# Kernel optimization log

Measured on AMD Instinct MI355X. Metric: run time of the kernel, lower is better.

The kernel has to match this reference:

```python
import jax, jax.numpy as jnp
import numpy as np

HIDDEN = 2048
N_HEADS = 16
N_KV_HEADS = 4
HEAD_DIM = HIDDEN // N_HEADS  # 128
N_GROUPS = N_HEADS // N_KV_HEADS  # 4
ROPE_THETA = 10000.0
B, S = 2, 2048


def setup_inputs() -> dict:
    key = jax.random.key(0)
    k1, k2, k3, k4, k5, k6 = jax.random.split(key, 6)
    hidden_states = jax.random.normal(k1, (B, S, HIDDEN), dtype=jnp.float32)
    position_ids = jnp.sort(jax.random.randint(k2, (B, S), 0, S), axis=-1).astype(jnp.int32)
    scale = 0.02
    Wq = jax.random.normal(k3, (HIDDEN, N_HEADS * HEAD_DIM), dtype=jnp.float32) * scale
    Wk = jax.random.normal(k4, (HIDDEN, N_KV_HEADS * HEAD_DIM), dtype=jnp.float32) * scale
    Wv = jax.random.normal(k5, (HIDDEN, N_KV_HEADS * HEAD_DIM), dtype=jnp.float32) * scale
    Wo = jax.random.normal(k6, (HIDDEN, HIDDEN), dtype=jnp.float32) * scale
    return {"hidden_states": hidden_states, "position_ids": position_ids,
            "Wq": Wq, "Wk": Wk, "Wv": Wv, "Wo": Wo}


def _rotate_half(x):
    x1, x2 = jnp.split(x, 2, axis=-1)
    return jnp.concatenate([-x2, x1], axis=-1)


def _rope_cos_sin(position_ids, dtype):
    # inv_freq: [HEAD_DIM/2]
    inv_freq = 1.0 / (ROPE_THETA ** (jnp.arange(0, HEAD_DIM, 2, dtype=jnp.float32) / HEAD_DIM))
    # freqs per position: [B, S, HEAD_DIM/2] -> duplicated to [B, S, HEAD_DIM]
    freqs = position_ids.astype(jnp.float32)[..., None] * inv_freq  # [B,S,Dh/2]
    emb = jnp.concatenate([freqs, freqs], axis=-1)  # [B,S,Dh]
    cos = jnp.cos(emb)[:, None, :, :].astype(dtype)  # [B,1,S,Dh]
    sin = jnp.sin(emb)[:, None, :, :].astype(dtype)
    return cos, sin


def reference(hidden_states, position_ids, Wq, Wk, Wv, Wo):
    b, s, _ = hidden_states.shape
    dtype = hidden_states.dtype
    q = (hidden_states @ Wq).reshape(b, s, N_HEADS, HEAD_DIM).transpose(0, 2, 1, 3)      # [B,Hq,S,Dh]
    k = (hidden_states @ Wk).reshape(b, s, N_KV_HEADS, HEAD_DIM).transpose(0, 2, 1, 3)   # [B,Hkv,S,Dh]
    v = (hidden_states @ Wv).reshape(b, s, N_KV_HEADS, HEAD_DIM).transpose(0, 2, 1, 3)

    cos, sin = _rope_cos_sin(position_ids, dtype)
    q = q * cos + _rotate_half(q) * sin
    k = k * cos + _rotate_half(k) * sin

    # repeat_kv: [B,Hkv,S,Dh] -> [B,Hq,S,Dh] (repeat-interleave along head axis)
    k = jnp.repeat(k, N_GROUPS, axis=1)
    v = jnp.repeat(v, N_GROUPS, axis=1)

    scores = jnp.einsum('bhqd,bhkd->bhqk', q, k) / jnp.sqrt(jnp.asarray(HEAD_DIM, dtype))
    # causal additive mask
    causal = jnp.tril(jnp.ones((s, s), dtype=bool))
    scores = jnp.where(causal[None, None], scores, jnp.asarray(-1e9, dtype))
    probs = jax.nn.softmax(scores, axis=-1)
    attn = jnp.einsum('bhqk,bhkd->bhqd', probs, v)  # [B,Hq,S,Dh]
    attn = attn.transpose(0, 2, 1, 3).reshape(b, s, HIDDEN)
    return attn @ Wo
```

## Files before the change

### kernel.cpp

```cpp
#include <hip/hip_runtime.h>
#include <math.h>

#define HID 2048
#define NH 16
#define NKV 4
#define DH 128
#define BB 2
#define SS 2048
#define ROWS (BB*SS)
#define NQKV 3072
#define KOFF 2048
#define VOFF 2560

typedef float f32x4 __attribute__((ext_vector_type(4)));
typedef __bf16 bf16x8 __attribute__((ext_vector_type(8)));
typedef unsigned short ushortx8 __attribute__((ext_vector_type(8)));
typedef unsigned short ushortx4 __attribute__((ext_vector_type(4)));
typedef float floatx4 __attribute__((ext_vector_type(4)));

__device__ __forceinline__ float b2f(unsigned short u) {
  union { float f; unsigned int i; } x; x.i = ((unsigned int)u) << 16; return x.f;
}
__device__ __forceinline__ unsigned short f2b(float f) {
  union { float f; unsigned int i; } x; x.f = f;
  unsigned int r = x.i + 0x7fffu + ((x.i >> 16) & 1u);
  return (unsigned short)(r >> 16);
}

__device__ __forceinline__ void gload16(const void* g, void* l) {
  __builtin_amdgcn_global_load_lds(
      (__attribute__((address_space(1))) void*)(void*)(g),
      (__attribute__((address_space(3))) void*)(l), 16, 0, 0);
}

__device__ __forceinline__ void wgbar() {
  asm volatile("" ::: "memory");
  __builtin_amdgcn_s_barrier();
  asm volatile("" ::: "memory");
}
#define VMCNT4 asm volatile("s_waitcnt vmcnt(4)" ::: "memory")
#define VMCNT0 asm volatile("s_waitcnt vmcnt(0)" ::: "memory")

__global__ __launch_bounds__(256) void cast_f32_bf16(const float* __restrict__ in,
                                                     unsigned short* __restrict__ out, int n4) {
  int i = blockIdx.x * 256 + threadIdx.x;
  if (i >= n4) return;
  floatx4 v = ((const floatx4*)in)[i];
  ushortx4 o;
  o.x = f2b(v.x); o.y = f2b(v.y); o.z = f2b(v.z); o.w = f2b(v.w);
  ((ushortx4*)out)[i] = o;
}

__global__ __launch_bounds__(256) void tcast(const float* __restrict__ W,
                                             unsigned short* __restrict__ Wt, int K, int N) {
  __shared__ float t[64][65];
  int tid = threadIdx.x;
  int k0 = blockIdx.y * 64, n0 = blockIdx.x * 64;
#pragma unroll
  for (int u0 = 0; u0 < 1024; u0 += 256) {
    int u = u0 + tid;
    int r = u >> 4, c4 = (u & 15) * 4;
    floatx4 v = *(const floatx4*)(const void*)&W[(size_t)(k0 + r) * N + n0 + c4];
    t[r][c4 + 0] = v.x; t[r][c4 + 1] = v.y; t[r][c4 + 2] = v.z; t[r][c4 + 3] = v.w;
  }
  __syncthreads();
#pragma unroll
  for (int u0 = 0; u0 < 512; u0 += 256) {
    int u = u0 + tid;
    int n = u >> 3, g = (u & 7) * 8;
    ushortx8 o;
#pragma unroll
    for (int k2 = 0; k2 < 8; ++k2) o[k2] = f2b(t[g + k2][n]);
    *(ushortx8*)(void*)&Wt[(size_t)(n0 + n) * K + k0 + g] = o;
  }
}

template <int BF16OUT>
__global__ __launch_bounds__(512, 1) void gemm256(const unsigned short* __restrict__ A,
                                                  const unsigned short* __restrict__ Bt,
                                                  void* __restrict__ Cv, int M, int N, int K) {
  __shared__ __align__(16) unsigned char smem[131072];
  const int tid = threadIdx.x;
  const int wave = tid >> 6, lane = tid & 63;
  const int fr = lane & 15, fq = lane >> 4;
  const int wm = wave >> 2, wn = wave & 3;

  const int ntn = N >> 8;
  const int cpx = gridDim.x >> 3;
  const int wg = (blockIdx.x & 7) * cpx + (blockIdx.x >> 3);
  const int m0 = (wg / ntn) << 8, n0 = (wg % ntn) << 8;
  const int NT = K >> 6;

  const int l8 = lane >> 3, l7 = lane & 7;
  const size_t srcOff = (size_t)(wave * 8 + l8) * K + ((l7 ^ l8) * 8);
  const unsigned short* Ag = A + (size_t)m0 * K;
  const unsigned short* Bg = Bt + (size_t)n0 * K;

  const int colx0 = (fq * 16) ^ ((fr & 7) << 4);
  const int colx1 = (64 + fq * 16) ^ ((fr & 7) << 4);
  const int aRow = (wm * 128 + fr) * 128;
  const int bRow = (wn * 64 + fr) * 128;

#define STAGE_A(kt2, mh)                                                                   \
  { const unsigned short* gp = Ag + (size_t)((mh) * 128) * K + (size_t)(kt2) * 64 + srcOff; \
    char* lp = (char*)smem + (((kt2) & 1) * 65536) + (mh) * 16384 + wave * 1024;            \
    gload16(gp, lp);                                                                        \
    gload16(gp + (size_t)64 * K, lp + 8192); }

#define STAGE_B(kt2, nh)                                                                   \
  { const unsigned short* gp = Bg + (size_t)((nh) * 128) * K + (size_t)(kt2) * 64 + srcOff; \
    char* lp = (char*)smem + (((kt2) & 1) * 65536) + 32768 + (nh) * 16384 + wave * 1024;    \
    gload16(gp, lp);                                                                        \
    gload16(gp + (size_t)64 * K, lp + 8192); }

  f32x4 acc[8][4] = {};
  bf16x8 aF[4][2], b0F[2][2], b1F[2][2];

#define LDA(mh)                                                                 \
  { const char* base_ = (const char*)smem + cur * 65536 + aRow;                 \
    _Pragma("unroll") for (int mi = 0; mi < 4; ++mi) {                          \
      aF[mi][0] = *(const bf16x8*)(const void*)(base_ + ((mh)*4 + mi) * 2048 + colx0); \
      aF[mi][1] = *(const bf16x8*)(const void*)(base_ + ((mh)*4 + mi) * 2048 + colx1); } }

#define LDB(nh, BF)                                                             \
  { const char* base_ = (const char*)smem + cur * 65536 + 32768 + bRow;         \
    _Pragma("unroll") for (int ni = 0; ni < 2; ++ni) {                          \
      BF[ni][0] = *(const bf16x8*)(const void*)(base_ + ((nh)*2 + ni) * 2048 + colx0); \
      BF[ni][1] = *(const bf16x8*)(const void*)(base_ + ((nh)*2 + ni) * 2048 + colx1); } }

#define MM(mh, nh, BF)                                                          \
  { __builtin_amdgcn_s_setprio(1);                                              \
    _Pragma("unroll") for (int mi = 0; mi < 4; ++mi)                            \
    _Pragma("unroll") for (int ni = 0; ni < 2; ++ni) {                          \
      acc[(mh)*4+mi][(nh)*2+ni] = __builtin_amdgcn_mfma_f32_16x16x32_bf16(      \
          aF[mi][0], BF[ni][0], acc[(mh)*4+mi][(nh)*2+ni], 0, 0, 0);            \
      acc[(mh)*4+mi][(nh)*2+ni] = __builtin_amdgcn_mfma_f32_16x16x32_bf16(      \
          aF[mi][1], BF[ni][1], acc[(mh)*4+mi][(nh)*2+ni], 0, 0, 0); }          \
    __builtin_amdgcn_s_setprio(0); }

  STAGE_A(0, 0); STAGE_A(0, 1); STAGE_B(0, 0); STAGE_B(0, 1);
  STAGE_B(1, 0); STAGE_B(1, 1);
  VMCNT4;
  wgbar();

  for (int kt = 0; kt < NT; ++kt) {
    const int cur = kt & 1;
    LDA(0); LDB(0, b0F);
    if (kt + 1 < NT) STAGE_A(kt + 1, 0);
    wgbar();
    MM(0, 0, b0F);
    wgbar();
    LDB(1, b1F);
    if (kt + 1 < NT) STAGE_A(kt + 1, 1);
    wgbar();
    MM(0, 1, b1F);
    wgbar();
    LDA(1);
    if (kt + 2 < NT) STAGE_B(kt + 2, 0);
    wgbar();
    MM(1, 0, b0F);
    wgbar();
    if (kt + 2 < NT) { STAGE_B(kt + 2, 1); VMCNT4; }
    else if (kt + 1 < NT) { VMCNT0; }
    wgbar();
    MM(1, 1, b1F);
    wgbar();
  }

#pragma unroll
  for (int mi = 0; mi < 8; ++mi)
#pragma unroll
    for (int ni = 0; ni < 4; ++ni)
#pragma unroll
      for (int r = 0; r < 4; ++r) {
        size_t row = (size_t)(m0 + wm * 128 + mi * 16 + fq * 4 + r);
        size_t col = (size_t)(n0 + wn * 64 + ni * 16 + fr);
        if (BF16OUT)
          ((unsigned short*)Cv)[row * N + col] = f2b(acc[mi][ni][r]);
        else
          ((float*)Cv)[row * N + col] = acc[mi][ni][r];
      }
#undef STAGE_A
#undef STAGE_B
#undef LDA
#undef LDB
#undef MM
}

template <int BF16OUT>
__global__ __launch_bounds__(512, 1) void gemm128n(const unsigned short* __restrict__ A,
                                                   const unsigned short* __restrict__ Bt,
                                                   void* __restrict__ Cv, int M, int N, int K) {
  __shared__ __align__(16) unsigned char smem[98304];
  const int tid = threadIdx.x;
  const int wave = tid >> 6, lane = tid & 63;
  const int fr = lane & 15, fq = lane >> 4;
  const int wm = wave & 3, wn = wave >> 2;

  const int ntn = N >> 8;
  const int cpx = gridDim.x >> 3;
  const int wg = (blockIdx.x & 7) * cpx + (blockIdx.x >> 3);
  const int m0 = (wg / ntn) << 7, n0 = (wg % ntn) << 8;
  const int NT = K >> 6;

  const int l8 = lane >> 3, l7 = lane & 7;
  const size_t srcOff = (size_t)(wave * 8 + l8) * K + ((l7 ^ l8) * 8);
  const unsigned short* Ag = A + (size_t)m0 * K;
  const unsigned short* Bg = Bt + (size_t)n0 * K;

  const int cx0 = (fq * 16) ^ ((fr & 7) << 4);
  const int cx1 = (64 + fq * 16) ^ ((fr & 7) << 4);
  const int aRow = (wm * 32 + fr) * 128;
  const int bRow = (wn * 128 + fr) * 128;

#define SA(kt2)  { const unsigned short* gp = Ag + (size_t)(kt2) * 64 + srcOff;             \
    char* lp = (char*)smem + (((kt2) & 1) * 49152) + wave * 1024;                           \
    gload16(gp, lp);  gload16(gp + (size_t)64 * K, lp + 8192); }
#define SB01(kt2) { const unsigned short* gp = Bg + (size_t)(kt2) * 64 + srcOff;            \
    char* lp = (char*)smem + (((kt2) & 1) * 49152) + 16384 + wave * 1024;                   \
    gload16(gp, lp);  gload16(gp + (size_t)64 * K, lp + 8192); }
#define SB23(kt2) { const unsigned short* gp = Bg + (size_t)128 * K + (size_t)(kt2) * 64 + srcOff; \
    char* lp = (char*)smem + (((kt2) & 1) * 49152) + 32768 + wave * 1024;                   \
    gload16(gp, lp);  gload16(gp + (size_t)64 * K, lp + 8192); }

  f32x4 acc[2][8] = {};
  bf16x8 aFk[2], bF0[4][2], bF1[4][2];

#define LDAK(kf) { const char* b_ = (const char*)smem + cur * 49152 + aRow;                 \
    aFk[0] = *(const bf16x8*)(const void*)(b_ + ((kf) ? cx1 : cx0));                        \
    aFk[1] = *(const bf16x8*)(const void*)(b_ + 2048 + ((kf) ? cx1 : cx0)); }
#define LDB4(BF, nb) { const char* b_ = (const char*)smem + cur * 49152 + 16384 + bRow + (nb) * 8192; \
    _Pragma("unroll") for (int ni = 0; ni < 4; ++ni) {                                      \
      BF[ni][0] = *(const bf16x8*)(const void*)(b_ + ni * 2048 + cx0);                      \
      BF[ni][1] = *(const bf16x8*)(const void*)(b_ + ni * 2048 + cx1); } }
#define MM8(BF, no, kf) { __builtin_amdgcn_s_setprio(1);                                    \
    _Pragma("unroll") for (int mi = 0; mi < 2; ++mi)                                        \
    _Pragma("unroll") for (int ni = 0; ni < 4; ++ni)                                        \
      acc[mi][(no) + ni] = __builtin_amdgcn_mfma_f32_16x16x32_bf16(                         \
          aFk[mi], BF[ni][kf], acc[mi][(no) + ni], 0, 0, 0);                                \
    __builtin_amdgcn_s_setprio(0); }

  SA(0); SB01(0); SB23(0); SB01(1); SB23(1);
  VMCNT4;
  wgbar();

  for (int kt = 0; kt < NT; ++kt) {
    const int cur = kt & 1;
    LDAK(0); LDB4(bF0, 0); LDB4(bF1, 1);
    if (kt + 1 < NT) SA(kt + 1);
    wgbar();
    MM8(bF0, 0, 0); MM8(bF1, 4, 0);
    wgbar();
    LDAK(1);
    if (kt + 2 < NT) { SB01(kt + 2); SB23(kt + 2); VMCNT4; }
    else if (kt + 1 < NT) { VMCNT0; }
    wgbar();
    MM8(bF0, 0, 1); MM8(bF1, 4, 1);
    wgbar();
  }

#pragma unroll
  for (int mi = 0; mi < 2; ++mi)
#pragma unroll
    for (int ni = 0; ni < 8; ++ni)
#pragma unroll
      for (int r = 0; r < 4; ++r) {
        size_t row = (size_t)(m0 + wm * 32 + mi * 16 + fq * 4 + r);
        size_t col = (size_t)(n0 + wn * 128 + ni * 16 + fr);
        if (BF16OUT)
          ((unsigned short*)Cv)[row * N + col] = f2b(acc[mi][ni][r]);
        else
          ((float*)Cv)[row * N + col] = acc[mi][ni][r];
      }
#undef SA
#undef SB01
#undef SB23
#undef LDAK
#undef LDB4
#undef MM8
}

__global__ __launch_bounds__(256) void rope_kernel(unsigned short* __restrict__ QKV,
                                                   const int* __restrict__ pos) {
  int bs = blockIdx.x;
  int t = threadIdx.x;
  __shared__ float cs[64], sn[64];
  if (t < 64) {
    float p = (float)pos[bs];
    float inv = expf(-(float)t * 0.14391156831212787f);
    sincosf(p * inv, &sn[t], &cs[t]);
  }
  __syncthreads();
  unsigned short* row = QKV + (size_t)bs * NQKV;
  for (int u = t; u < 320; u += 256) {
    int h = u >> 4, d0 = (u & 15) * 4;
    int col = (h < 16) ? h * DH : KOFF + (h - 16) * DH;
    float sc = (h < 16) ? 0.08838834764831845f : 1.0f;
    ushortx4 lo = *(const ushortx4*)(const void*)(row + col + d0);
    ushortx4 hi = *(const ushortx4*)(const void*)(row + col + 64 + d0);
    ushortx4 olo, ohi;
#pragma unroll
    for (int k = 0; k < 4; ++k) {
      float x1 = b2f(lo[k]), x2 = b2f(hi[k]);
      float c = cs[d0 + k], s = sn[d0 + k];
      olo[k] = f2b((x1 * c - x2 * s) * sc);
      ohi[k] = f2b((x2 * c + x1 * s) * sc);
    }
    *(ushortx4*)(void*)(row + col + d0) = olo;
    *(ushortx4*)(void*)(row + col + 64 + d0) = ohi;
  }
}

__global__ __launch_bounds__(256) void vtrans(const unsigned short* __restrict__ QKV,
                                              unsigned short* __restrict__ Vt) {
  __shared__ unsigned short t[32][34];
  int s0 = blockIdx.x * 32, d0 = blockIdx.y * 32;
  int bh = blockIdx.z; int b = bh >> 2, h = bh & 3;
  int tx = threadIdx.x & 31, ty = threadIdx.x >> 5;
  const unsigned short* src = QKV + (size_t)b * SS * NQKV + VOFF + h * DH;
  for (int i = 0; i < 32; i += 8)
    t[ty + i][tx] = src[(size_t)(s0 + ty + i) * NQKV + d0 + tx];
  __syncthreads();
  unsigned short* dst = Vt + ((size_t)(b * NKV + h) * DH) * SS;
  for (int i = 0; i < 32; i += 8)
    dst[(size_t)(d0 + ty + i) * SS + s0 + tx] = t[tx][ty + i];
}

__global__ __launch_bounds__(512, 2) void attn_kernel(const unsigned short* __restrict__ QKV,
                                                      const unsigned short* __restrict__ Vt,
                                                      unsigned short* __restrict__ Out) {
  int id = blockIdx.x;
  int g = id & 7;
  int b = g >> 2, hkv = g & 3;
  int r3 = id >> 3;
  int h = hkv * 4 + (r3 & 3);
  int qt = 15 - (r3 >> 2);
  int tid = threadIdx.x;
  int wave = tid >> 6, lane = tid & 63;
  int fr = lane & 15, fq = lane >> 4;
  __shared__ __align__(16) unsigned short K_lds[2][64 * 128];
  __shared__ __align__(16) unsigned short V_lds[2][128 * 64];
  __shared__ __align__(16) unsigned short P_lds[8][16 * 64];

  int krow = tid >> 4, kcc = tid & 15;
  int vrow = tid >> 3, vcc = tid & 7;
  const unsigned short* Kbase = QKV + (size_t)b * SS * NQKV + KOFF + hkv * DH;
  const unsigned short* Vbase = Vt + (size_t)(b * NKV + hkv) * DH * SS;
  char* pbase = (char*)&P_lds[wave][0];

  const unsigned short* Qp =
      QKV + (size_t)((size_t)b * SS + qt * 128 + wave * 16 + fr) * NQKV + h * DH;
  bf16x8 qf[4];
#pragma unroll
  for (int i = 0; i < 4; ++i) qf[i] = *(const bf16x8*)(const void*)(Qp + i * 32 + fq * 8);

  f32x4 o[8] = {};
  float lsum[4] = {0.f, 0.f, 0.f, 0.f};
  ushortx8 KR[2], VR[2];

#define PREF(kv0)                                                                          \
  { KR[0] = *(const ushortx8*)(const void*)(Kbase + (size_t)((kv0) + krow) * NQKV + kcc * 8);      \
    KR[1] = *(const ushortx8*)(const void*)(Kbase + (size_t)((kv0) + krow + 32) * NQKV + kcc * 8); \
    VR[0] = *(const ushortx8*)(const void*)(Vbase + (size_t)vrow * SS + (kv0) + vcc * 8);          \
    VR[1] = *(const ushortx8*)(const void*)(Vbase + (size_t)(vrow + 64) * SS + (kv0) + vcc * 8); }

#define WRITE(buf)                                                                         \
  { *(ushortx8*)(void*)((char*)K_lds[buf] + krow * 256 + ((kcc * 16) ^ ((krow & 7) << 4))) = KR[0]; \
    *(ushortx8*)(void*)((char*)K_lds[buf] + (krow + 32) * 256 + ((kcc * 16) ^ ((krow & 7) << 4))) = KR[1]; \
    *(ushortx8*)(void*)((char*)V_lds[buf] + vrow * 128 + ((vcc * 16) ^ ((vrow & 7) << 4))) = VR[0]; \
    *(ushortx8*)(void*)((char*)V_lds[buf] + (vrow + 64) * 128 + ((vcc * 16) ^ ((vrow & 7) << 4))) = VR[1]; }

  int nt = 2 * qt + 2;
  PREF(0); WRITE(0);
  __syncthreads();
  int cur = 0;

  for (int t = 0; t < nt; ++t) {
    int havenext = (t + 1 < nt);
    if (havenext) PREF((t + 1) * 64);

    f32x4 sf[4];
    __builtin_amdgcn_s_setprio(1);
#pragma unroll
    for (int n = 0; n < 4; ++n) {
      f32x4 acc = {};
      int kc = n * 16 + fr;
      const char* kr = (const char*)K_lds[cur] + kc * 256;
#pragma unroll
      for (int kf = 0; kf < 4; ++kf) {
        bf16x8 kfr = *(const bf16x8*)(const void*)(kr + (((kf * 32 + fq * 8) * 2) ^ ((kc & 7) << 4)));
        acc = __builtin_amdgcn_mfma_f32_16x16x32_bf16(qf[kf], kfr, acc, 0, 0, 0);
      }
      sf[n] = acc;
    }
    __builtin_amdgcn_s_setprio(0);
    if (t >= 2 * qt) {
#pragma unroll
      for (int n = 0; n < 4; ++n)
#pragma unroll
        for (int r = 0; r < 4; ++r) {
          int kvc = t * 64 + n * 16 + fr, qr = qt * 128 + wave * 16 + fq * 4 + r;
          if (kvc > qr) sf[n][r] = -1e30f;
        }
    }
#pragma unroll
    for (int n = 0; n < 4; ++n)
#pragma unroll
      for (int r = 0; r < 4; ++r) sf[n][r] = __expf(sf[n][r]);
#pragma unroll
    for (int r = 0; r < 4; ++r)
      lsum[r] += (sf[0][r] + sf[1][r]) + (sf[2][r] + sf[3][r]);
#pragma unroll
    for (int n = 0; n < 4; ++n)
#pragma unroll
      for (int r = 0; r < 4; ++r) {
        int prow = fq * 4 + r, pcol = n * 16 + fr;
        *(unsigned short*)(pbase + prow * 128 + ((pcol * 2) ^ ((prow & 7) << 4))) = f2b(sf[n][r]);
      }
    __builtin_amdgcn_s_setprio(1);
#pragma unroll
    for (int kf2 = 0; kf2 < 2; ++kf2) {
      bf16x8 pa = *(const bf16x8*)(const void*)(pbase + fr * 128 + (((kf2 * 32 + fq * 8) * 2) ^ ((fr & 7) << 4)));
#pragma unroll
      for (int df = 0; df < 8; ++df) {
        int dc = df * 16 + fr;
        bf16x8 vb = *(const bf16x8*)(const void*)((const char*)V_lds[cur] + dc * 128 + (((kf2 * 32 + fq * 8) * 2) ^ ((dc & 7) << 4)));
        o[df] = __builtin_amdgcn_mfma_f32_16x16x32_bf16(pa, vb, o[df], 0, 0, 0);
      }
    }
    __builtin_amdgcn_s_setprio(0);

    if (havenext) WRITE(cur ^ 1);
    __syncthreads();
    cur ^= 1;
  }
#undef PREF
#undef WRITE

#pragma unroll
  for (int r = 0; r < 4; ++r) {
    float s = lsum[r];
    s += __shfl_xor(s, 1); s += __shfl_xor(s, 2);
    s += __shfl_xor(s, 4); s += __shfl_xor(s, 8);
    float inv = 1.0f / s;
    size_t orow = (size_t)((size_t)b * SS + qt * 128 + wave * 16 + fq * 4 + r) * HID + h * DH;
#pragma unroll
    for (int df = 0; df < 8; ++df)
      Out[orow + df * 16 + fr] = f2b(o[df][r] * inv);
  }
}

extern "C" void kernel_launch(void* const* d_in, const int* in_sizes, int n_in,
                              void* d_out, int out_size, void* d_ws, size_t ws_size,
                              hipStream_t stream) {
  const float* hs = (const float*)d_in[0];
  const int* pos = (const int*)d_in[1];
  const float* Wq = (const float*)d_in[2];
  const float* Wk = (const float*)d_in[3];
  const float* Wv = (const float*)d_in[4];
  const float* Wo = (const float*)d_in[5];

  char* ws = (char*)d_ws;
  size_t off = 0;
  unsigned short* hsb = (unsigned short*)(ws + off); off += (size_t)ROWS * HID * 2;
  unsigned short* WqkvT = (unsigned short*)(ws + off); off += (size_t)NQKV * HID * 2;
  unsigned short* WoT = (unsigned short*)(ws + off); off += (size_t)HID * HID * 2;
  unsigned short* QKV = (unsigned short*)(ws + off); off += (size_t)ROWS * NQKV * 2;
  unsigned short* Vtb = (unsigned short*)(ws + off); off += (size_t)BB * NKV * DH * SS * 2;

  cast_f32_bf16<<<(ROWS * HID / 4 + 255) / 256, 256, 0, stream>>>(hs, hsb, ROWS * HID / 4);
  tcast<<<dim3(HID / 64, HID / 64), 256, 0, stream>>>(Wq, WqkvT, HID, HID);
  tcast<<<dim3(512 / 64, HID / 64), 256, 0, stream>>>(Wk, WqkvT + (size_t)2048 * 2048, HID, 512);
  tcast<<<dim3(512 / 64, HID / 64), 256, 0, stream>>>(Wv, WqkvT + (size_t)2560 * 2048, HID, 512);
  tcast<<<dim3(HID / 64, HID / 64), 256, 0, stream>>>(Wo, WoT, HID, HID);

  gemm256<1><<<(ROWS / 256) * (NQKV / 256), 512, 0, stream>>>(hsb, WqkvT, QKV, ROWS, NQKV, HID);
  rope_kernel<<<ROWS, 256, 0, stream>>>(QKV, pos);
  vtrans<<<dim3(SS / 32, DH / 32, BB * NKV), 256, 0, stream>>>(QKV, Vtb);
  attn_kernel<<<512, 512, 0, stream>>>(QKV, Vtb, hsb);
  gemm128n<0><<<(ROWS / 128) * (HID / 256), 512, 0, stream>>>(hsb, WoT, d_out, ROWS, HID, HID);
}
```

Baseline: 203.3 us.

## Rewrite attention with 32x32 MFMA, register-resident P and direct-to-LDS loads

The attention kernel moves from 16x16x32 to 32x32x16 bf16 MFMAs, with 4 waves of 32 query rows each instead of 8 waves of 16. It computes S transposed (K as the A operand), so the probabilities stay in registers and are repacked with cvt_pk and a cross-half shuffle instead of a round trip through P_lds. K/V staging now uses global_load_lds with swizzled source addresses, removing the register staging and LDS write pass. Q tiles are interleaved across blocks to balance causal work. The cost is higher register pressure and fewer threads per block to hide latency.

```diff
diff --git a/kernel.cpp b/kernel.cpp
--- a/kernel.cpp
+++ b/kernel.cpp
@@ -13,6 +13,7 @@
 #define VOFF 2560
 
 typedef float f32x4 __attribute__((ext_vector_type(4)));
+typedef float f32x16 __attribute__((ext_vector_type(16)));
 typedef __bf16 bf16x8 __attribute__((ext_vector_type(8)));
 typedef unsigned short ushortx8 __attribute__((ext_vector_type(8)));
 typedef unsigned short ushortx4 __attribute__((ext_vector_type(4)));
@@ -40,6 +41,12 @@
 }
 #define VMCNT4 asm volatile("s_waitcnt vmcnt(4)" ::: "memory")
 #define VMCNT0 asm volatile("s_waitcnt vmcnt(0)" ::: "memory")
+
+__device__ __forceinline__ unsigned cvtpk(float lo, float hi_) {
+  unsigned r;
+  asm("v_cvt_pk_bf16_f32 %0, %1, %2" : "=v"(r) : "v"(lo), "v"(hi_));
+  return r;
+}
 
 __global__ __launch_bounds__(256) void cast_f32_bf16(const float* __restrict__ in,
                                                      unsigned short* __restrict__ out, int n4) {
@@ -326,127 +333,153 @@
     dst[(size_t)(d0 + ty + i) * SS + s0 + tx] = t[tx][ty + i];
 }
 
-__global__ __launch_bounds__(512, 2) void attn_kernel(const unsigned short* __restrict__ QKV,
+__global__ __launch_bounds__(256, 2) void attn_kernel(const unsigned short* __restrict__ QKV,
                                                       const unsigned short* __restrict__ Vt,
                                                       unsigned short* __restrict__ Out) {
   int id = blockIdx.x;
   int g = id & 7;
   int b = g >> 2, hkv = g & 3;
   int r3 = id >> 3;
-  int h = hkv * 4 + (r3 & 3);
-  int qt = 15 - (r3 >> 2);
+  int h = hkv * 4 + (r3 >> 4);
+  int j = r3 & 15;
+  int qt = (j & 1) ? (j >> 1) : (15 - (j >> 1));
   int tid = threadIdx.x;
-  int wave = tid >> 6, lane = tid & 63;
-  int fr = lane & 15, fq = lane >> 4;
+  int w = tid >> 6, lane = tid & 63;
+  int l31 = lane & 31, hi = lane >> 5;
+
   __shared__ __align__(16) unsigned short K_lds[2][64 * 128];
   __shared__ __align__(16) unsigned short V_lds[2][128 * 64];
-  __shared__ __align__(16) unsigned short P_lds[8][16 * 64];
-
-  int krow = tid >> 4, kcc = tid & 15;
-  int vrow = tid >> 3, vcc = tid & 7;
+  __shared__ float lsum_lds[4][32];
+
   const unsigned short* Kbase = QKV + (size_t)b * SS * NQKV + KOFF + hkv * DH;
   const unsigned short* Vbase = Vt + (size_t)(b * NKV + hkv) * DH * SS;
-  char* pbase = (char*)&P_lds[wave][0];
+
+  int kr4 = lane >> 4, kc = lane & 15;
+  int vr8 = lane >> 3, vc = lane & 7;
+
+#define STAGE(kv0, buf)                                                                  \
+  { _Pragma("unroll") for (int i = 0; i < 4; ++i) {                                      \
+      int r0 = w * 16 + i * 4; int row = r0 + kr4;                                       \
+      gload16(Kbase + (size_t)((kv0) + row) * NQKV + ((kc ^ (row & 7)) * 8),             \
+              (char*)K_lds[buf] + r0 * 256); }                                           \
+    _Pragma("unroll") for (int i = 0; i < 4; ++i) {                                      \
+      int r0 = w * 32 + i * 8; int row = r0 + vr8;                                       \
+      gload16(Vbase + (size_t)row * SS + (kv0) + ((vc ^ (row & 7)) * 8),                 \
+              (char*)V_lds[buf] + r0 * 128); } }
 
   const unsigned short* Qp =
-      QKV + (size_t)((size_t)b * SS + qt * 128 + wave * 16 + fr) * NQKV + h * DH;
-  bf16x8 qf[4];
-#pragma unroll
-  for (int i = 0; i < 4; ++i) qf[i] = *(const bf16x8*)(const void*)(Qp + i * 32 + fq * 8);
-
-  f32x4 o[8] = {};
-  float lsum[4] = {0.f, 0.f, 0.f, 0.f};
-  ushortx8 KR[2], VR[2];
-
-#define PREF(kv0)                                                                          \
-  { KR[0] = *(const ushortx8*)(const void*)(Kbase + (size_t)((kv0) + krow) * NQKV + kcc * 8);      \
-    KR[1] = *(const ushortx8*)(const void*)(Kbase + (size_t)((kv0) + krow + 32) * NQKV + kcc * 8); \
-    VR[0] = *(const ushortx8*)(const void*)(Vbase + (size_t)vrow * SS + (kv0) + vcc * 8);          \
-    VR[1] = *(const ushortx8*)(const void*)(Vbase + (size_t)(vrow + 64) * SS + (kv0) + vcc * 8); }
-
-#define WRITE(buf)                                                                         \
-  { *(ushortx8*)(void*)((char*)K_lds[buf] + krow * 256 + ((kcc * 16) ^ ((krow & 7) << 4))) = KR[0]; \
-    *(ushortx8*)(void*)((char*)K_lds[buf] + (krow + 32) * 256 + ((kcc * 16) ^ ((krow & 7) << 4))) = KR[1]; \
-    *(ushortx8*)(void*)((char*)V_lds[buf] + vrow * 128 + ((vcc * 16) ^ ((vrow & 7) << 4))) = VR[0]; \
-    *(ushortx8*)(void*)((char*)V_lds[buf] + (vrow + 64) * 128 + ((vcc * 16) ^ ((vrow & 7) << 4))) = VR[1]; }
-
+      QKV + (size_t)((size_t)b * SS + qt * 128 + w * 32 + l31) * NQKV + h * DH + hi * 8;
+  bf16x8 qf[8];
+#pragma unroll
+  for (int ks = 0; ks < 8; ++ks) qf[ks] = *(const bf16x8*)(const void*)(Qp + ks * 16);
+
+  f32x16 o[4] = {};
+  float lsum = 0.f;
+  int lsw = (l31 & 7) << 4;
   int nt = 2 * qt + 2;
-  PREF(0); WRITE(0);
-  __syncthreads();
+
+  STAGE(0, 0);
+  VMCNT0;
+  wgbar();
   int cur = 0;
 
   for (int t = 0; t < nt; ++t) {
-    int havenext = (t + 1 < nt);
-    if (havenext) PREF((t + 1) * 64);
-
-    f32x4 sf[4];
+    if (t + 1 < nt) STAGE((t + 1) * 64, cur ^ 1);
+
+    f32x16 s0 = {}, s1 = {};
+    {
+      const char* kb = (const char*)K_lds[cur];
+      __builtin_amdgcn_s_setprio(1);
+#pragma unroll
+      for (int ks = 0; ks < 8; ++ks) {
+        int co = (ks * 32 + hi * 16) ^ lsw;
+        bf16x8 k0 = *(const bf16x8*)(const void*)(kb + l31 * 256 + co);
+        bf16x8 k1 = *(const bf16x8*)(const void*)(kb + (32 + l31) * 256 + co);
+        s0 = __builtin_amdgcn_mfma_f32_32x32x16_bf16(k0, qf[ks], s0, 0, 0, 0);
+        s1 = __builtin_amdgcn_mfma_f32_32x32x16_bf16(k1, qf[ks], s1, 0, 0, 0);
+      }
+      __builtin_amdgcn_s_setprio(0);
+    }
+
+    float p0[16], p1[16];
+    float ps = 0.f;
+    if (t >= 2 * qt) {
+      int qrel = w * 32 + l31 - (t - 2 * qt) * 64;
+#pragma unroll
+      for (int r = 0; r < 16; ++r) {
+        int kvr = (r & 3) + 8 * (r >> 2) + 4 * hi;
+        float e0 = __expf(s0[r]), e1 = __expf(s1[r]);
+        p0[r] = (kvr <= qrel) ? e0 : 0.f;
+        p1[r] = (kvr + 32 <= qrel) ? e1 : 0.f;
+        ps += p0[r] + p1[r];
+      }
+    } else {
+#pragma unroll
+      for (int r = 0; r < 16; ++r) {
+        p0[r] = __expf(s0[r]); p1[r] = __expf(s1[r]);
+        ps += p0[r] + p1[r];
+      }
+    }
+    lsum += ps;
+
+    union U8 { unsigned u[4]; bf16x8 v; } fa[4];
+    {
+      unsigned a0 = cvtpk(p0[0], p0[1]),  a1 = cvtpk(p0[2], p0[3]);
+      unsigned a2 = cvtpk(p0[4], p0[5]),  a3 = cvtpk(p0[6], p0[7]);
+      unsigned sa0 = __shfl_xor(a0, 32), sa1 = __shfl_xor(a1, 32);
+      unsigned sa2 = __shfl_xor(a2, 32), sa3 = __shfl_xor(a3, 32);
+      fa[0].u[0] = hi ? sa2 : a0;  fa[0].u[1] = hi ? sa3 : a1;
+      fa[0].u[2] = hi ? a2 : sa0;  fa[0].u[3] = hi ? a3 : sa1;
+      unsigned a4 = cvtpk(p0[8], p0[9]),   a5 = cvtpk(p0[10], p0[11]);
+      unsigned a6 = cvtpk(p0[12], p0[13]), a7 = cvtpk(p0[14], p0[15]);
+      unsigned sa4 = __shfl_xor(a4, 32), sa5 = __shfl_xor(a5, 32);
+      unsigned sa6 = __shfl_xor(a6, 32), sa7 = __shfl_xor(a7, 32);
+      fa[1].u[0] = hi ? sa6 : a4;  fa[1].u[1] = hi ? sa7 : a5;
+      fa[1].u[2] = hi ? a6 : sa4;  fa[1].u[3] = hi ? a7 : sa5;
+      unsigned b0 = cvtpk(p1[0], p1[1]),  b1 = cvtpk(p1[2], p1[3]);
+      unsigned b2 = cvtpk(p1[4], p1[5]),  b3 = cvtpk(p1[6], p1[7]);
+      unsigned sb0 = __shfl_xor(b0, 32), sb1 = __shfl_xor(b1, 32);
+      unsigned sb2 = __shfl_xor(b2, 32), sb3 = __shfl_xor(b3, 32);
+      fa[2].u[0] = hi ? sb2 : b0;  fa[2].u[1] = hi ? sb3 : b1;
+      fa[2].u[2] = hi ? b2 : sb0;  fa[2].u[3] = hi ? b3 : sb1;
+      unsigned b4 = cvtpk(p1[8], p1[9]),   b5 = cvtpk(p1[10], p1[11]);
+      unsigned b6 = cvtpk(p1[12], p1[13]), b7 = cvtpk(p1[14], p1[15]);
+      unsigned sb4 = __shfl_xor(b4, 32), sb5 = __shfl_xor(b5, 32);
+      unsigned sb6 = __shfl_xor(b6, 32), sb7 = __shfl_xor(b7, 32);
+      fa[3].u[0] = hi ? sb6 : b4;  fa[3].u[1] = hi ? sb7 : b5;
+      fa[3].u[2] = hi ? b6 : sb4;  fa[3].u[3] = hi ? b7 : sb5;
+    }
+
     __builtin_amdgcn_s_setprio(1);
 #pragma unroll
-    for (int n = 0; n < 4; ++n) {
-      f32x4 acc = {};
-      int kc = n * 16 + fr;
-      const char* kr = (const char*)K_lds[cur] + kc * 256;
-#pragma unroll
-      for (int kf = 0; kf < 4; ++kf) {
-        bf16x8 kfr = *(const bf16x8*)(const void*)(kr + (((kf * 32 + fq * 8) * 2) ^ ((kc & 7) << 4)));
-        acc = __builtin_amdgcn_mfma_f32_16x16x32_bf16(qf[kf], kfr, acc, 0, 0, 0);
-      }
-      sf[n] = acc;
-    }
-    __builtin_amdgcn_s_setprio(0);
-    if (t >= 2 * qt) {
-#pragma unroll
-      for (int n = 0; n < 4; ++n)
-#pragma unroll
-        for (int r = 0; r < 4; ++r) {
-          int kvc = t * 64 + n * 16 + fr, qr = qt * 128 + wave * 16 + fq * 4 + r;
-          if (kvc > qr) sf[n][r] = -1e30f;
-        }
-    }
-#pragma unroll
-    for (int n = 0; n < 4; ++n)
-#pragma unroll
-      for (int r = 0; r < 4; ++r) sf[n][r] = __expf(sf[n][r]);
-#pragma unroll
-    for (int r = 0; r < 4; ++r)
-      lsum[r] += (sf[0][r] + sf[1][r]) + (sf[2][r] + sf[3][r]);
-#pragma unroll
-    for (int n = 0; n < 4; ++n)
-#pragma unroll
-      for (int r = 0; r < 4; ++r) {
-        int prow = fq * 4 + r, pcol = n * 16 + fr;
-        *(unsigned short*)(pbase + prow * 128 + ((pcol * 2) ^ ((prow & 7) << 4))) = f2b(sf[n][r]);
-      }
-    __builtin_amdgcn_s_setprio(1);
-#pragma unroll
-    for (int kf2 = 0; kf2 < 2; ++kf2) {
-      bf16x8 pa = *(const bf16x8*)(const void*)(pbase + fr * 128 + (((kf2 * 32 + fq * 8) * 2) ^ ((fr & 7) << 4)));
-#pragma unroll
-      for (int df = 0; df < 8; ++df) {
-        int dc = df * 16 + fr;
-        bf16x8 vb = *(const bf16x8*)(const void*)((const char*)V_lds[cur] + dc * 128 + (((kf2 * 32 + fq * 8) * 2) ^ ((dc & 7) << 4)));
-        o[df] = __builtin_amdgcn_mfma_f32_16x16x32_bf16(pa, vb, o[df], 0, 0, 0);
+    for (int dblk = 0; dblk < 4; ++dblk) {
+      const char* vrow = (const char*)V_lds[cur] + (dblk * 32 + l31) * 128;
+#pragma unroll
+      for (int ks = 0; ks < 4; ++ks) {
+        bf16x8 vb = *(const bf16x8*)(const void*)(vrow + ((ks * 32 + hi * 16) ^ lsw));
+        o[dblk] = __builtin_amdgcn_mfma_f32_32x32x16_bf16(fa[ks].v, vb, o[dblk], 0, 0, 0);
       }
     }
     __builtin_amdgcn_s_setprio(0);
 
-    if (havenext) WRITE(cur ^ 1);
-    __syncthreads();
+    VMCNT0;
+    wgbar();
     cur ^= 1;
   }
-#undef PREF
-#undef WRITE
-
-#pragma unroll
-  for (int r = 0; r < 4; ++r) {
-    float s = lsum[r];
-    s += __shfl_xor(s, 1); s += __shfl_xor(s, 2);
-    s += __shfl_xor(s, 4); s += __shfl_xor(s, 8);
-    float inv = 1.0f / s;
-    size_t orow = (size_t)((size_t)b * SS + qt * 128 + wave * 16 + fq * 4 + r) * HID + h * DH;
-#pragma unroll
-    for (int df = 0; df < 8; ++df)
-      Out[orow + df * 16 + fr] = f2b(o[df][r] * inv);
+#undef STAGE
+
+  float ls = lsum + __shfl_xor(lsum, 32);
+  if (hi == 0) lsum_lds[w][l31] = ls;
+  __syncthreads();
+  size_t obase = (size_t)((size_t)b * SS + qt * 128 + w * 32) * HID + h * DH + l31;
+#pragma unroll
+  for (int r = 0; r < 16; ++r) {
+    int qr = (r & 3) + 8 * (r >> 2) + 4 * hi;
+    float inv = 1.0f / lsum_lds[w][qr];
+    size_t orow = obase + (size_t)qr * HID;
+#pragma unroll
+    for (int dblk = 0; dblk < 4; ++dblk)
+      Out[orow + dblk * 32] = f2b(o[dblk][r] * inv);
   }
 }
 
@@ -477,6 +510,6 @@
   gemm256<1><<<(ROWS / 256) * (NQKV / 256), 512, 0, stream>>>(hsb, WqkvT, QKV, ROWS, NQKV, HID);
   rope_kernel<<<ROWS, 256, 0, stream>>>(QKV, pos);
   vtrans<<<dim3(SS / 32, DH / 32, BB * NKV), 256, 0, stream>>>(QKV, Vtb);
-  attn_kernel<<<512, 512, 0, stream>>>(QKV, Vtb, hsb);
+  attn_kernel<<<512, 256, 0, stream>>>(QKV, Vtb, hsb);
   gemm128n<0><<<(ROWS / 128) * (HID / 256), 512, 0, stream>>>(hsb, WoT, d_out, ROWS, HID, HID);
 }
```

After: 216.7 us. 6.6% more time.
